# Optimization experiments

Hardware: AMD Instinct MI355X
Metric: run time of the kernel (lower is better)

## Reference

```python
import jax, jax.numpy as jnp
import numpy as np

N_NODES = 4096
N_EDGES = 65536
N_FEAT = 128
HIDDEN = 64
N_FILT = 8


def setup_inputs() -> dict:
    key = jax.random.key(0)
    k1, k2, k3, k4, k5, k6 = jax.random.split(key, 6)
    X = jax.random.normal(k1, (N_NODES, N_FEAT), dtype=jnp.float32)
    edge_list = jax.random.randint(k2, (2, N_EDGES), 0, N_NODES)
    W1 = jax.random.normal(k3, (N_FEAT, HIDDEN), dtype=jnp.float32) / np.sqrt(N_FEAT)
    b1 = jax.random.normal(k4, (HIDDEN,), dtype=jnp.float32) * 0.01
    W2 = jax.random.normal(k5, (HIDDEN, N_FILT), dtype=jnp.float32) / np.sqrt(HIDDEN)
    b2 = jax.random.normal(k6, (N_FILT,), dtype=jnp.float32) * 0.01
    return {"X": X, "edge_list": edge_list, "W1": W1, "b1": b1, "W2": W2, "b2": b2}


def _diagram0(vals, adj):
    """0-dim persistence of one filtration via incremental union-find.

    Faithful to the torch code: nodes are inserted in ascending filtration
    order; when node v (sorted rank j) is inserted, it is connected to every
    already-present in-neighbor u (edge u->v in edge_list). A component's
    root is its member with minimal rank (what DFS-over-sorted-order picks as
    component[0]). A root born at step b that loses root status at step d has
    longevity (b, d-1); roots alive at the end get (b, inf).
    Returns (pairs [n,2], born_mask [n]) indexed by rank; masked rows are the
    entries the torch dict would contain, in the same (insertion) order.
    """
    n = vals.shape[0]
    order = jnp.argsort(vals)          # node id at each rank
    rank = jnp.argsort(order)          # rank of each node id
    ranks = jnp.arange(n)

    def step(carry, j):
        root, alive, death = carry     # root[node] -> root rank; alive/death indexed by rank
        v = order[j]
        nbr = adj[v] & (rank < j)                      # present in-neighbors of v
        cand = jnp.where(nbr, root, j)                 # roots to merge (j for non-nbrs)
        m = jnp.min(cand)                              # elder root (min rank) of merged comp
        merged = jnp.zeros(n, dtype=bool).at[cand].set(True)
        dies = merged & alive & (ranks != m)           # younger roots die now
        death = jnp.where(dies, (j - 1).astype(jnp.float32), death)
        alive = (alive & ~dies).at[j].set(m == j)      # v is born as a root iff isolated
        root = jnp.where(merged[root], m, root)
        return (root, alive, death), None

    init = (rank, jnp.zeros(n, dtype=bool), jnp.full(n, jnp.inf, dtype=jnp.float32))
    (root, alive, death), _ = jax.lax.scan(step, init, jnp.arange(n))
    born = alive | jnp.isfinite(death)                 # ranks that ever were roots
    pairs = jnp.stack([ranks.astype(jnp.float32), death], axis=1)  # (birth, death)
    return pairs, born


def reference(X, edge_list, W1, b1, W2, b2):
    n = X.shape[0]
    # filtrations = Linear -> ReLU -> Linear
    filt = jnp.maximum(X @ W1 + b1, 0.0) @ W2 + b2     # [n, n_filtrations]
    src, tgt = edge_list[0], edge_list[1]
    adj = jnp.zeros((n, n), dtype=bool).at[tgt, src].set(True)  # adj[v,u]: edge u->v
    pairs, mask = jax.vmap(lambda v: _diagram0(v, adj))(filt.T)
    return pairs, mask  # [F, n, 2] persistence pairs + [F, n] validity mask
```

## Files before the change

### kernel.cpp

```cpp
#include <hip/hip_runtime.h>
#include <hip/hip_bf16.h>
#include <cmath>

static constexpr int NN = 4096;
static constexpr int NE = 65536;
static constexpr int NF = 128;
static constexpr int NH = 64;
static constexpr int NQ = 8;
static constexpr int ECAP = 4096;

static constexpr float DEATH_SENTINEL_F = 3.3895313892515355e38f;

__global__ __launch_bounds__(256) void tg_mlp(const float* __restrict__ X,
                                              const float* __restrict__ W1,
                                              const float* __restrict__ b1,
                                              const float* __restrict__ W2,
                                              const float* __restrict__ b2,
                                              float* __restrict__ filt)
{
    __shared__ float sW1[NF * NH];
    __shared__ float sW2[NH * NQ];
    __shared__ float sb1[NH];
    __shared__ float sb2[NQ];
    const int tid = threadIdx.x;
    for (int i = tid; i < NF * NH; i += 256) sW1[i] = W1[i];
    for (int i = tid; i < NH * NQ; i += 256) sW2[i] = W2[i];
    if (tid < NH) sb1[tid] = b1[tid];
    if (tid < NQ) sb2[tid] = b2[tid];
    __syncthreads();

    const int node = blockIdx.x * 256 + tid;
    const float* xrow = X + (size_t)node * NF;

    double acc[NH];
#pragma unroll
    for (int h = 0; h < NH; ++h) acc[h] = (double)sb1[h];

    for (int k0 = 0; k0 < NF; k0 += 8) {
        float xv[8];
#pragma unroll
        for (int kk = 0; kk < 8; ++kk) xv[kk] = xrow[k0 + kk];
#pragma unroll
        for (int kk = 0; kk < 8; ++kk) {
            const float* wrow = &sW1[(k0 + kk) * NH];
            const double xd = (double)xv[kk];
#pragma unroll
            for (int h = 0; h < NH; ++h) acc[h] += xd * (double)wrow[h];
        }
    }
    double o[NQ];
#pragma unroll
    for (int f = 0; f < NQ; ++f) o[f] = (double)sb2[f];
#pragma unroll
    for (int h = 0; h < NH; ++h) {
        const float hv = fmaxf((float)acc[h], 0.0f);
        const double hd = (double)hv;
#pragma unroll
        for (int f = 0; f < NQ; ++f) o[f] += hd * (double)sW2[h * NQ + f];
    }
#pragma unroll
    for (int f = 0; f < NQ; ++f) filt[node * NQ + f] = (float)o[f];
}

__global__ __launch_bounds__(1024) void tg_sort(const float* __restrict__ filt,
                                                int* __restrict__ rankv)
{
    const int f = blockIdx.x;
    const int tid = threadIdx.x;
    __shared__ float sv[NN];
    __shared__ int   si[NN];
    for (int i = tid; i < NN; i += 1024) { sv[i] = filt[i * NQ + f]; si[i] = i; }
    __syncthreads();
    for (int k = 2; k <= NN; k <<= 1) {
        for (int j = k >> 1; j > 0; j >>= 1) {
            for (int i = tid; i < NN; i += 1024) {
                const int l = i ^ j;
                if (l > i) {
                    const float a = sv[i], b = sv[l];
                    const int ia = si[i], ib = si[l];
                    const bool up = ((i & k) == 0);
                    const bool agtb = (a > b) || (a == b && ia > ib);
                    if (up ? agtb : !agtb) {
                        sv[i] = b; sv[l] = a; si[i] = ib; si[l] = ia;
                    }
                }
            }
            __syncthreads();
        }
    }
    for (int j2 = tid; j2 < NN; j2 += 1024) {
        rankv[f * NN + si[j2]] = j2;
    }
}

__global__ void tg_rzero(int* __restrict__ rdeg, int* __restrict__ rcursor)
{
    const int i = blockIdx.x * 256 + threadIdx.x;
    if (i < NQ * NN) { rdeg[i] = 0; rcursor[i] = 0; }
}

__global__ void tg_rhist(const int* __restrict__ srcn, const int* __restrict__ tgt,
                         const int* __restrict__ rankv, int* __restrict__ rdeg)
{
    const int e = blockIdx.x * 256 + threadIdx.x;
    if (e >= NE) return;
    const int u = srcn[e], v = tgt[e];
#pragma unroll
    for (int f = 0; f < NQ; ++f) {
        const int rs = rankv[f * NN + u];
        const int rt = rankv[f * NN + v];
        if (rs < rt) atomicAdd(&rdeg[f * NN + rt], 1);
    }
}

__global__ __launch_bounds__(1024) void tg_rscan(const int* __restrict__ rdeg, int* __restrict__ rstarts)
{
    const int f = blockIdx.x;
    const int* in = rdeg + f * NN;
    int* outp = rstarts + f * (NN + 1);
    __shared__ int bufA[NN];
    __shared__ int bufB[NN];
    const int tid = threadIdx.x;
    for (int i = tid; i < NN; i += 1024) bufA[i] = in[i];
    __syncthreads();
    int* s = bufA;
    int* d = bufB;
    for (int off = 1; off < NN; off <<= 1) {
        for (int i = tid; i < NN; i += 1024) d[i] = s[i] + ((i >= off) ? s[i - off] : 0);
        __syncthreads();
        int* t = s; s = d; d = t;
    }
    for (int i = tid; i < NN; i += 1024) outp[i + 1] = s[i];
    if (tid == 0) outp[0] = 0;
}

__global__ void tg_rscatter(const int* __restrict__ srcn, const int* __restrict__ tgt,
                            const int* __restrict__ rankv, const int* __restrict__ rstarts,
                            int* __restrict__ rcursor, unsigned short* __restrict__ rcsr16)
{
    const int e = blockIdx.x * 256 + threadIdx.x;
    if (e >= NE) return;
    const int u = srcn[e], v = tgt[e];
#pragma unroll
    for (int f = 0; f < NQ; ++f) {
        const int rs = rankv[f * NN + u];
        const int rt = rankv[f * NN + v];
        if (rs < rt) {
            const int pos = rstarts[f * (NN + 1) + rt] + atomicAdd(&rcursor[f * NN + rt], 1);
            rcsr16[(size_t)f * NE + pos] = (unsigned short)rs;
        }
    }
}

__device__ __forceinline__ int wave_min_i32(int m)
{
    m = min(m, __builtin_amdgcn_update_dpp(0x7fffffff, m, 0x111, 0xF, 0xF, false));
    m = min(m, __builtin_amdgcn_update_dpp(0x7fffffff, m, 0x112, 0xF, 0xF, false));
    m = min(m, __builtin_amdgcn_update_dpp(0x7fffffff, m, 0x114, 0xF, 0xF, false));
    m = min(m, __builtin_amdgcn_update_dpp(0x7fffffff, m, 0x118, 0xF, 0xF, false));
    m = min(m, __builtin_amdgcn_update_dpp(0x7fffffff, m, 0x142, 0xF, 0xF, false));
    m = min(m, __builtin_amdgcn_update_dpp(0x7fffffff, m, 0x143, 0xF, 0xF, false));
    return __builtin_amdgcn_readlane(m, 63);
}

__global__ __launch_bounds__(256) void tg_uf(const int* __restrict__ rstarts,
                                             const unsigned short* __restrict__ rcsr16,
                                             __hip_bfloat16* __restrict__ out)
{
    const int f = blockIdx.x;
    const int t = threadIdx.x;
    const int lane = t & 63;
    const int wid = t >> 6;
    __shared__ int parent[NN];
    __shared__ int death[NN];
    __shared__ unsigned short ebuf[2][ECAP];
    __shared__ unsigned char sflag3[2][3][64];

    const unsigned short* grcsr = rcsr16 + (size_t)f * NE;
    const int* rrow = rstarts + f * (NN + 1);

    for (int i = t; i < NN; i += 256) { parent[i] = i; death[i] = 0x7fffffff; }
    __syncthreads();

    volatile int* vparent = parent;

    for (int it = 0; it <= 64; ++it) {
        if (wid == 0) {
            if (it > 0) {
                const int w  = it - 1;
                const int j0 = w * 64;
                const int b  = w & 1;
                const int rs  = rrow[j0 + lane];
                const int rs2 = rrow[j0 + lane + 1];
                const int deg = rs2 - rs;
                const int s0w    = __shfl(rs, 0);
                const int wcount = __shfl(rs2, 63) - s0w;
                if (wcount <= ECAP) {
                    const int off = rs - s0w;
                    const bool flag = (deg > 0) &&
                        ((sflag3[b][0][lane] | sflag3[b][1][lane] | sflag3[b][2][lane]) != 0);
                    if (deg > 0 && !flag) parent[j0 + lane] = (int)ebuf[b][off];
                    unsigned long long imask = __ballot(flag);
                    while (imask) {
                        const int jj = __builtin_ctzll(imask);
                        imask &= imask - 1;
                        const int j   = j0 + jj;
                        const int sof = __shfl(off, jj);
                        const int dj  = __shfl(deg, jj);
                        int rmin = 0x7fffffff;
                        for (int e = lane; e < dj; e += 64) {
                            int x = (int)ebuf[b][sof + e];
                            int p = parent[x];
                            while (p != x) { const int g = parent[p]; parent[x] = g; x = g; p = parent[x]; }
                            rmin = min(rmin, x);
                        }
                        const int m = wave_min_i32(rmin);
                        for (int e = lane; e < dj; e += 64) {
                            int x = (int)ebuf[b][sof + e];
                            int p = parent[x];
                            while (p != x) { x = p; p = parent[x]; }
                            if (x != m) { death[x] = j - 1; parent[x] = m; }
                        }
                        if (lane == 0) parent[j] = m;
                    }
                } else {
                    for (int jj = 0; jj < 64; ++jj) {
                        const int j  = j0 + jj;
                        const int sj = __shfl(rs, jj);
                        const int dj = __shfl(deg, jj);
                        if (dj == 0) continue;
                        int rmin = 0x7fffffff;
                        for (int e = lane; e < dj; e += 64) {
                            int x = (int)grcsr[sj + e];
                            int p = parent[x];
                            while (p != x) { const int g = parent[p]; parent[x] = g; x = g; p = parent[x]; }
                            rmin = min(rmin, x);
                        }
                        const int m = wave_min_i32(rmin);
                        for (int e = lane; e < dj; e += 64) {
                            int x = (int)grcsr[sj + e];
                            int p = parent[x];
                            while (p != x) { x = p; p = parent[x]; }
                            if (x != m) { death[x] = j - 1; parent[x] = m; }
                        }
                        if (lane == 0) parent[j] = m;
                    }
                }
            }
        } else {
            if (it < 64) {
                const int w    = it;
                const int j0   = w * 64;
                const int bb   = w & 1;
                const int part = wid - 1;
                const int jj   = lane;
                const int sA   = rrow[j0 + jj];
                const int sB   = rrow[j0 + jj + 1];
                const int s0w  = rrow[j0];
                const int wcount = rrow[j0 + 64] - s0w;
                if (wcount <= ECAP) {
                    const int deg = sB - sA;
                    const int off = sA - s0w;
                    bool diff = false;
                    if (deg > 0) {
                        int x0 = (int)grcsr[sA];
                        int p0 = vparent[x0];
                        while (p0 != x0) { x0 = p0; p0 = vparent[x0]; }
                        const int c0 = x0;
                        if (part == 0) ebuf[bb][off] = (unsigned short)c0;
                        for (int e = (part == 0 ? 3 : part); e < deg; e += 3) {
                            int x = (int)grcsr[sA + e];
                            int p = vparent[x];
                            while (p != x) { x = p; p = vparent[x]; }
                            ebuf[bb][off + e] = (unsigned short)x;
                            diff |= (x != c0);
                        }
                    }
                    sflag3[bb][part][jj] = diff ? 1 : 0;
                }
            }
        }
        __syncthreads();
    }

    __hip_bfloat16* pairs = out;
    __hip_bfloat16* masko = out + NQ * NN * 2;
    const __hip_bfloat16 bsent = __float2bfloat16(DEATH_SENTINEL_F);
    for (int i = t; i < NN; i += 256) {
        const int d = death[i];
        const int degi = rrow[i + 1] - rrow[i];
        pairs[(f * NN + i) * 2 + 0] = __float2bfloat16((float)i);
        pairs[(f * NN + i) * 2 + 1] = (d == 0x7fffffff) ? bsent : __float2bfloat16((float)d);
        const bool bornm = (degi == 0) || (d != 0x7fffffff);
        masko[f * NN + i] = __float2bfloat16(bornm ? 1.0f : 0.0f);
    }
}

extern "C" void kernel_launch(void* const* d_in, const int* in_sizes, int n_in,
                              void* d_out, int out_size, void* d_ws, size_t ws_size,
                              hipStream_t stream)
{
    const float* X  = (const float*)d_in[0];
    const int* edges = (const int*)d_in[1];
    const float* W1 = (const float*)d_in[2];
    const float* b1 = (const float*)d_in[3];
    const float* W2 = (const float*)d_in[4];
    const float* b2 = (const float*)d_in[5];
    __hip_bfloat16* out = (__hip_bfloat16*)d_out;

    char* ws = (char*)d_ws;
    float* filt            = (float*)(ws + 0);
    int* rankv             = (int*)(ws + 131072);
    int* rdeg              = (int*)(ws + 262144);
    int* rcursor           = (int*)(ws + 393216);
    int* rstarts           = (int*)(ws + 524288);
    unsigned short* rcsr16 = (unsigned short*)(ws + 655424);

    const int* srcn = edges;
    const int* tgt  = edges + NE;

    tg_mlp<<<NN / 256, 256, 0, stream>>>(X, W1, b1, W2, b2, filt);
    tg_sort<<<NQ, 1024, 0, stream>>>(filt, rankv);
    tg_rzero<<<(NQ * NN) / 256, 256, 0, stream>>>(rdeg, rcursor);
    tg_rhist<<<NE / 256, 256, 0, stream>>>(srcn, tgt, rankv, rdeg);
    tg_rscan<<<NQ, 1024, 0, stream>>>(rdeg, rstarts);
    tg_rscatter<<<NE / 256, 256, 0, stream>>>(srcn, tgt, rankv, rstarts, rcursor, rcsr16);
    tg_uf<<<NQ, 256, 0, stream>>>(rstarts, rcsr16, out);
}
```

Before: 717.1 us.

## Rebalance union-find pipeline: flat prefetch of edge roots, serial wave re-resolves

The three helper waves now resolve edge sources to roots over a flat, coalesced range of the next 64-node window instead of splitting per node, and the per-node flag array is dropped. The serial wave re-resolves each prefetched root against the current parent array (with path compression) and computes the all-same-root test itself. Single-chunk merges (degree up to 64) take a one-pass path. Row starts are cached in LDS and ECAP is shrunk to make room. This shifts some pointer chasing onto the critical serial wave, and windows larger than 3072 edges fall back to the slow path more often.

```diff
diff --git a/kernel.cpp b/kernel.cpp
--- a/kernel.cpp
+++ b/kernel.cpp
@@ -7,7 +7,7 @@
 static constexpr int NF = 128;
 static constexpr int NH = 64;
 static constexpr int NQ = 8;
-static constexpr int ECAP = 4096;
+static constexpr int ECAP = 3072;
 
 static constexpr float DEATH_SENTINEL_F = 3.3895313892515355e38f;
 
@@ -173,13 +173,14 @@
     const int wid = t >> 6;
     __shared__ int parent[NN];
     __shared__ int death[NN];
+    __shared__ int sstarts[NN + 1];
     __shared__ unsigned short ebuf[2][ECAP];
-    __shared__ unsigned char sflag3[2][3][64];
 
     const unsigned short* grcsr = rcsr16 + (size_t)f * NE;
     const int* rrow = rstarts + f * (NN + 1);
 
     for (int i = t; i < NN; i += 256) { parent[i] = i; death[i] = 0x7fffffff; }
+    for (int i = t; i < NN + 1; i += 256) sstarts[i] = rrow[i];
     __syncthreads();
 
     volatile int* vparent = parent;
@@ -190,36 +191,64 @@
                 const int w  = it - 1;
                 const int j0 = w * 64;
                 const int b  = w & 1;
-                const int rs  = rrow[j0 + lane];
-                const int rs2 = rrow[j0 + lane + 1];
+                const int rs  = sstarts[j0 + lane];
+                const int rs2 = sstarts[j0 + lane + 1];
                 const int deg = rs2 - rs;
                 const int s0w    = __shfl(rs, 0);
                 const int wcount = __shfl(rs2, 63) - s0w;
                 if (wcount <= ECAP) {
                     const int off = rs - s0w;
-                    const bool flag = (deg > 0) &&
-                        ((sflag3[b][0][lane] | sflag3[b][1][lane] | sflag3[b][2][lane]) != 0);
-                    if (deg > 0 && !flag) parent[j0 + lane] = (int)ebuf[b][off];
-                    unsigned long long imask = __ballot(flag);
+                    int c0 = -1;
+                    bool diff = false;
+                    for (int e = 0; e < deg; ++e) {
+                        int x = (int)ebuf[b][off + e];
+                        int p = parent[x];
+                        if (p != x) {
+                            int r = p, q = parent[r];
+                            while (q != r) { r = q; q = parent[r]; }
+                            parent[x] = r;
+                            p = r;
+                        }
+                        ebuf[b][off + e] = (unsigned short)p;
+                        if (e == 0) c0 = p; else diff |= (p != c0);
+                    }
+                    if (deg > 0 && !diff) parent[j0 + lane] = c0;
+                    unsigned long long imask = __ballot(deg > 0 && diff);
                     while (imask) {
                         const int jj = __builtin_ctzll(imask);
                         imask &= imask - 1;
                         const int j   = j0 + jj;
                         const int sof = __shfl(off, jj);
                         const int dj  = __shfl(deg, jj);
-                        int rmin = 0x7fffffff;
-                        for (int e = lane; e < dj; e += 64) {
-                            int x = (int)ebuf[b][sof + e];
-                            int p = parent[x];
-                            while (p != x) { const int g = parent[p]; parent[x] = g; x = g; p = parent[x]; }
-                            rmin = min(rmin, x);
-                        }
-                        const int m = wave_min_i32(rmin);
-                        for (int e = lane; e < dj; e += 64) {
-                            int x = (int)ebuf[b][sof + e];
-                            int p = parent[x];
-                            while (p != x) { x = p; p = parent[x]; }
-                            if (x != m) { death[x] = j - 1; parent[x] = m; }
+                        int m;
+                        if (dj <= 64) {
+                            int rfin = 0x7fffffff;
+                            if (lane < dj) {
+                                int x = (int)ebuf[b][sof + lane];
+                                int p = parent[x];
+                                while (p != x) { x = p; p = parent[x]; }
+                                rfin = x;
+                            }
+                            m = wave_min_i32(rfin);
+                            if (lane < dj && rfin != m) {
+                                death[rfin] = j - 1;
+                                parent[rfin] = m;
+                            }
+                        } else {
+                            int rmin = 0x7fffffff;
+                            for (int e = lane; e < dj; e += 64) {
+                                int x = (int)ebuf[b][sof + e];
+                                int p = parent[x];
+                                while (p != x) { x = p; p = parent[x]; }
+                                rmin = min(rmin, x);
+                            }
+                            m = wave_min_i32(rmin);
+                            for (int e = lane; e < dj; e += 64) {
+                                int x = (int)ebuf[b][sof + e];
+                                int p = parent[x];
+                                while (p != x) { x = p; p = parent[x]; }
+                                if (x != m) { death[x] = j - 1; parent[x] = m; }
+                            }
                         }
                         if (lane == 0) parent[j] = m;
                     }
@@ -249,34 +278,17 @@
             }
         } else {
             if (it < 64) {
-                const int w    = it;
-                const int j0   = w * 64;
-                const int bb   = w & 1;
-                const int part = wid - 1;
-                const int jj   = lane;
-                const int sA   = rrow[j0 + jj];
-                const int sB   = rrow[j0 + jj + 1];
-                const int s0w  = rrow[j0];
-                const int wcount = rrow[j0 + 64] - s0w;
+                const int j0   = it * 64;
+                const int bb   = it & 1;
+                const int s0w  = sstarts[j0];
+                const int wcount = sstarts[j0 + 64] - s0w;
                 if (wcount <= ECAP) {
-                    const int deg = sB - sA;
-                    const int off = sA - s0w;
-                    bool diff = false;
-                    if (deg > 0) {
-                        int x0 = (int)grcsr[sA];
-                        int p0 = vparent[x0];
-                        while (p0 != x0) { x0 = p0; p0 = vparent[x0]; }
-                        const int c0 = x0;
-                        if (part == 0) ebuf[bb][off] = (unsigned short)c0;
-                        for (int e = (part == 0 ? 3 : part); e < deg; e += 3) {
-                            int x = (int)grcsr[sA + e];
-                            int p = vparent[x];
-                            while (p != x) { x = p; p = vparent[x]; }
-                            ebuf[bb][off + e] = (unsigned short)x;
-                            diff |= (x != c0);
-                        }
-                    }
-                    sflag3[bb][part][jj] = diff ? 1 : 0;
+                    for (int k = (wid - 1) * 64 + lane; k < wcount; k += 192) {
+                        int x = (int)grcsr[s0w + k];
+                        int p = vparent[x];
+                        while (p != x) { x = p; p = vparent[x]; }
+                        ebuf[bb][k] = (unsigned short)x;
+                    }
                 }
             }
         }
@@ -288,7 +300,7 @@
     const __hip_bfloat16 bsent = __float2bfloat16(DEATH_SENTINEL_F);
     for (int i = t; i < NN; i += 256) {
         const int d = death[i];
-        const int degi = rrow[i + 1] - rrow[i];
+        const int degi = sstarts[i + 1] - sstarts[i];
         pairs[(f * NN + i) * 2 + 0] = __float2bfloat16((float)i);
         pairs[(f * NN + i) * 2 + 1] = (d == 0x7fffffff) ? bsent : __float2bfloat16((float)d);
         const bool bornm = (degi == 0) || (d != 0x7fffffff);
```

Result: faster. 631.6 us (-11.9%).
